# Kernel tuning notes

Hardware: AMD Instinct MI355X
Metric: run time of the kernel (lower is better)

## Reference

```python
import jax, jax.numpy as jnp
import numpy as np

B, S, D, H = 2, 2048, 1024, 16
HD = D // H

def setup_inputs() -> dict:
    key = jax.random.key(0)
    ks = jax.random.split(key, 11)
    s = 1.0 / np.sqrt(D)
    return {
        "query": jax.random.normal(ks[0], (B, S, D), jnp.float32),
        "key": jax.random.normal(ks[1], (B, S, D), jnp.float32),
        "value": jax.random.normal(ks[2], (B, S, D), jnp.float32),
        "Wq": jax.random.normal(ks[3], (D, D), jnp.float32) * s,
        "bq": jax.random.normal(ks[4], (D,), jnp.float32) * s,
        "Wk": jax.random.normal(ks[5], (D, D), jnp.float32) * s,
        "bk": jax.random.normal(ks[6], (D,), jnp.float32) * s,
        "Wv": jax.random.normal(ks[7], (D, D), jnp.float32) * s,
        "bv": jax.random.normal(ks[8], (D,), jnp.float32) * s,
        "Wo": jax.random.normal(ks[9], (D, D), jnp.float32) * s,
        "bo": jax.random.normal(ks[10], (D,), jnp.float32) * s,
        "test": 0,
    }

def _heads(x, W, b):
    # [B,S,D] @ [D,D] -> [B,S,D] -> [B,H,S,HD]
    y = x @ W + b
    return y.reshape(B, -1, H, HD).transpose(0, 2, 1, 3)

def reference(query, key, value, Wq, bq, Wk, bk, Wv, bv, Wo, bo, test):
    q = _heads(query, Wq, bq)
    k = _heads(key, Wk, bk)
    v = _heads(value, Wv, bv)
    scale = 1.0 / np.sqrt(HD).astype(np.float32)
    scores = jnp.einsum('bhqd,bhkd->bhqk', q, k) * scale  # [B,H,S,S]
    if test:
        return scores
    prob = jax.nn.softmax(scores, axis=-1)
    out = jnp.einsum('bhqk,bhkd->bhqd', prob, v)
    out = out.transpose(0, 2, 1, 3).reshape(B, -1, D)
    return out @ Wo + bo
```

## Files before the change

### kernel.cpp

```cpp
#include <hip/hip_runtime.h>

constexpr int Bn  = 2;
constexpr int Sn  = 2048;
constexpr int Dn  = 1024;
constexpr int Hn  = 16;
constexpr int HDn = 64;
constexpr int Mn  = Bn * Sn;

typedef _Float16 half8 __attribute__((ext_vector_type(8)));
typedef _Float16 half4 __attribute__((ext_vector_type(4)));
typedef float    f32x4 __attribute__((ext_vector_type(4)));

__device__ __forceinline__ void cp16(const _Float16* g, _Float16* l) {
  __builtin_amdgcn_global_load_lds(
      (__attribute__((address_space(1))) void*)g,
      (__attribute__((address_space(3))) void*)l, 16, 0, 0);
}

__global__ __launch_bounds__(256) void prep_kernel(
    const float* __restrict__ q, const float* __restrict__ k,
    const float* __restrict__ v,
    const float* __restrict__ Wq, const float* __restrict__ Wk,
    const float* __restrict__ Wv, const float* __restrict__ Wo,
    _Float16* __restrict__ Xh, _Float16* __restrict__ WT) {
  __shared__ float tile[64][65];
  const int n = blockIdx.x;
  const int tid = threadIdx.x;
  if (n < 12288) {
    const int z = n >> 12;
    const float* src = (z == 0) ? q : (z == 1) ? k : v;
    _Float16* dst = Xh + (size_t)z * (Mn * Dn);
    int i = (n & 4095) * 256 + tid;
    float4 v4 = ((const float4*)src)[i];
    half4 h;
    h.x = (_Float16)v4.x; h.y = (_Float16)v4.y;
    h.z = (_Float16)v4.z; h.w = (_Float16)v4.w;
    *(half4*)(dst + (size_t)i * 4) = h;
  } else {
    const int m = n - 12288;
    const int z = m >> 8, rem = m & 255;
    const float* W = (z == 0) ? Wq : (z == 1) ? Wk : (z == 2) ? Wv : Wo;
    _Float16* T = WT + (size_t)z * Dn * Dn;
    const int k0 = (rem >> 4) * 64, n0 = (rem & 15) * 64;
#pragma unroll
    for (int i = 0; i < 4; i++) {
      int s = tid + i * 256;
      int r = s >> 4, c4 = s & 15;
      float4 w4 = *(const float4*)(W + (size_t)(k0 + r) * Dn + n0 + c4 * 4);
      tile[r][c4 * 4 + 0] = w4.x; tile[r][c4 * 4 + 1] = w4.y;
      tile[r][c4 * 4 + 2] = w4.z; tile[r][c4 * 4 + 3] = w4.w;
    }
    __syncthreads();
#pragma unroll
    for (int i = 0; i < 2; i++) {
      int s = tid + i * 256;
      int nn = s >> 3, r8 = (s & 7) * 8;
      half8 h;
#pragma unroll
      for (int j = 0; j < 8; j++) h[j] = (_Float16)tile[r8 + j][nn];
      *(half8*)(T + (size_t)(n0 + nn) * Dn + k0 + r8) = h;
    }
  }
}

__global__ __launch_bounds__(256) void proj_kernel(
    const _Float16* __restrict__ Xh, const _Float16* __restrict__ WT,
    const float* __restrict__ bq, const float* __restrict__ bk,
    const float* __restrict__ bv,
    _Float16* __restrict__ Qh, _Float16* __restrict__ Kh,
    _Float16* __restrict__ VT) {
  const int z = blockIdx.z;
  const _Float16* A  = Xh + (size_t)z * Mn * Dn;
  const _Float16* Bm = WT + (size_t)z * Dn * Dn;
  const float* bias = (z == 0) ? bq : (z == 1) ? bk : bv;

  __shared__ __align__(16) _Float16 smem[2 * 128 * 64];
  _Float16* As = smem;
  _Float16* Bs = smem + 128 * 64;

  const int tid  = threadIdx.x;
  const int lane = tid & 63;
  const int w    = tid >> 6;
  const int wm   = (w >> 1) * 64;
  const int wn   = (w & 1) * 64;
  const int m0   = blockIdx.y * 128;
  const int n0   = blockIdx.x * 128;
  const int qd   = lane >> 4;
  const int lm   = lane & 15;

  const int st_r = tid >> 3;
  const int st_u = (tid & 7) ^ (st_r & 7);

  f32x4 acc[4][4];
#pragma unroll
  for (int i = 0; i < 4; i++)
#pragma unroll
    for (int j = 0; j < 4; j++) acc[i][j] = {0.f, 0.f, 0.f, 0.f};

  for (int k0 = 0; k0 < Dn; k0 += 64) {
#pragma unroll
    for (int p = 0; p < 4; p++) {
      int row = st_r + p * 32;
      cp16(A + (size_t)(m0 + row) * Dn + k0 + st_u * 8, As + (tid + p * 256) * 8);
      cp16(Bm + (size_t)(n0 + row) * Dn + k0 + st_u * 8, Bs + (tid + p * 256) * 8);
    }
    __syncthreads();
#pragma unroll
    for (int ks = 0; ks < 2; ks++) {
      const int up = ((ks * 4 + qd) ^ (lm & 7)) * 8;
      half8 a[4], bb[4];
#pragma unroll
      for (int mi = 0; mi < 4; mi++)
        a[mi] = *(const half8*)(As + (wm + mi * 16 + lm) * 64 + up);
#pragma unroll
      for (int ni = 0; ni < 4; ni++)
        bb[ni] = *(const half8*)(Bs + (wn + ni * 16 + lm) * 64 + up);
      if (z < 2) {
#pragma unroll
        for (int mi = 0; mi < 4; mi++)
#pragma unroll
          for (int ni = 0; ni < 4; ni++)
            acc[mi][ni] = __builtin_amdgcn_mfma_f32_16x16x32_f16(bb[ni], a[mi], acc[mi][ni], 0, 0, 0);
      } else {
#pragma unroll
        for (int mi = 0; mi < 4; mi++)
#pragma unroll
          for (int ni = 0; ni < 4; ni++)
            acc[mi][ni] = __builtin_amdgcn_mfma_f32_16x16x32_f16(a[mi], bb[ni], acc[mi][ni], 0, 0, 0);
      }
    }
    __syncthreads();
  }

  char* T = (char*)smem;
  const int b_ = m0 >> 11, s0 = m0 & (Sn - 1), h0 = n0 >> 6;

  if (z < 2) {
    _Float16* out = (z == 0) ? Qh : Kh;
    const float scl = (z == 0) ? 0.125f * 1.44269504089f : 1.0f;
#pragma unroll
    for (int mi = 0; mi < 4; mi++) {
      int tok = wm + mi * 16 + lm;
#pragma unroll
      for (int ni = 0; ni < 4; ni++) {
        int feat = wn + ni * 16 + qd * 4;
        float4 b4 = *(const float4*)(bias + n0 + feat);
        half4 h4;
        h4[0] = (_Float16)((acc[mi][ni][0] + b4.x) * scl);
        h4[1] = (_Float16)((acc[mi][ni][1] + b4.y) * scl);
        h4[2] = (_Float16)((acc[mi][ni][2] + b4.z) * scl);
        h4[3] = (_Float16)((acc[mi][ni][3] + b4.w) * scl);
        *(half4*)(T + tok * 256 + ((feat * 2) ^ ((tok & 7) << 4))) = h4;
      }
    }
    __syncthreads();
#pragma unroll
    for (int i = 0; i < 8; i++) {
      int slot = tid + i * 256;
      int r = slot >> 3, c16 = slot & 7;
      int hh = r >> 7, sm = r & 127;
      half8 v8 = *(const half8*)(T + sm * 256 + ((hh * 128 + c16 * 16) ^ ((sm & 7) << 4)));
      *(half8*)(out + (((size_t)(b_ * Hn + h0 + hh)) * Sn + s0 + sm) * HDn + c16 * 8) = v8;
    }
  } else {
#pragma unroll
    for (int ni = 0; ni < 4; ni++) {
      int feat = wn + ni * 16 + lm;
      float b_f = bias[n0 + feat];
#pragma unroll
      for (int mi = 0; mi < 4; mi++) {
        int tk = wm + mi * 16 + qd * 4;
        half4 h4;
#pragma unroll
        for (int r = 0; r < 4; r++) h4[r] = (_Float16)(acc[mi][ni][r] + b_f);
        *(half4*)(T + feat * 256 + ((tk * 2) ^ ((feat & 7) << 4))) = h4;
      }
    }
    __syncthreads();
#pragma unroll
    for (int i = 0; i < 8; i++) {
      int slot = tid + i * 256;
      int f = slot >> 4, c16 = slot & 15;
      half8 v8 = *(const half8*)(T + f * 256 + ((c16 * 16) ^ ((f & 7) << 4)));
      int head = h0 + (f >> 6), hd = f & 63;
      *(half8*)(VT + (((size_t)(b_ * Hn + head)) * HDn + hd) * Sn + s0 + c16 * 8) = v8;
    }
  }
}

__global__ __launch_bounds__(256, 2) void attn_kernel(
    const _Float16* __restrict__ Qh, const _Float16* __restrict__ Kh,
    const _Float16* __restrict__ VT, _Float16* __restrict__ attn_out) {
  __shared__ __align__(16) _Float16 Ksb[2][128 * 64];
  __shared__ __align__(16) _Float16 Vsb[2][64 * 128];
  __shared__ __align__(16) _Float16 Ps[4 * 32 * 64];

  const int n    = blockIdx.x;
  const int slot = n >> 3;
  const int bh   = (n & 7) * 4 + (slot >> 4);
  const int q0   = (slot & 15) * 128;
  const size_t base = (size_t)bh * Sn * HDn;

  const int tid  = threadIdx.x;
  const int lane = tid & 63;
  const int w    = tid >> 6;
  const int qd   = lane >> 4;
  const int lm   = lane & 15;

  const _Float16* qptr = Qh + base + (size_t)(q0 + w * 32 + lm) * HDn + qd * 8;
  half8 qa[2][2];
#pragma unroll
  for (int nj = 0; nj < 2; nj++)
#pragma unroll
    for (int ks = 0; ks < 2; ks++)
      qa[nj][ks] = *(const half8*)(qptr + nj * 16 * HDn + ks * 32);

  half8 vones;
#pragma unroll
  for (int j = 0; j < 8; j++) vones[j] = (lm == 0) ? (_Float16)1.0f : (_Float16)0.0f;

  f32x4 oacc[2][4];
#pragma unroll
  for (int i = 0; i < 2; i++)
#pragma unroll
    for (int j = 0; j < 4; j++) oacc[i][j] = {0.f, 0.f, 0.f, 0.f};
  f32x4 oaccl[2] = {{0.f, 0.f, 0.f, 0.f}, {0.f, 0.f, 0.f, 0.f}};

  char* Psw = (char*)(Ps + w * (32 * 64));
  const f32x4 sinit = {-10.f, -10.f, -10.f, -10.f};

  const int st_r = tid >> 3;
  const int st_u = (tid & 7) ^ (st_r & 7);
  const _Float16* kbase = Kh + base;
  const _Float16* vbase = VT + base;

#define STAGE_K(KT, DST)                                                     \
  {                                                                          \
    const _Float16* src_ = kbase + (size_t)(KT) * 128 * HDn;                 \
    _Float16* dst_ = (DST);                                                  \
    _Pragma("unroll")                                                        \
    for (int p = 0; p < 4; p++)                                              \
      cp16(src_ + (size_t)(st_r + p * 32) * HDn + st_u * 8,                  \
           dst_ + (tid + p * 256) * 8);                                      \
  }

#define STAGE_V(KT, DST)                                                     \
  {                                                                          \
    _Float16* dst_ = (DST);                                                  \
    _Pragma("unroll")                                                        \
    for (int p = 0; p < 4; p++) {                                            \
      int s_ = tid + p * 256;                                                \
      int r_ = s_ >> 4, u_ = (s_ & 15) ^ (r_ & 15);                          \
      cp16(vbase + (size_t)r_ * Sn + (KT) * 128 + u_ * 8, dst_ + s_ * 8);    \
    }                                                                        \
  }

#define LOAD_V(C, VB)                                                        \
  _Pragma("unroll")                                                          \
  for (int oi = 0; oi < 4; oi++)                                             \
    _Pragma("unroll")                                                        \
    for (int k2 = 0; k2 < 2; k2++)                                           \
      VB[oi][k2] = *(const half8*)(Vsb[cur] +                                \
          ((oi * 16 + lm) * 16 + (((C) * 8 + k2 * 4 + qd) ^ lm)) * 8);

#define QK(C, SACC)                                                          \
  {                                                                          \
    _Pragma("unroll")                                                        \
    for (int n4 = 0; n4 < 4; n4++)                                           \
      _Pragma("unroll")                                                      \
      for (int nj = 0; nj < 2; nj++) SACC[n4][nj] = sinit;                   \
    __builtin_amdgcn_s_setprio(1);                                           \
    _Pragma("unroll")                                                        \
    for (int n4 = 0; n4 < 4; n4++) {                                         \
      int ni = 4 * (C) + n4;                                                 \
      _Pragma("unroll")                                                      \
      for (int ks = 0; ks < 2; ks++) {                                       \
        int up = (4 * ks + qd) ^ (lm & 7);                                   \
        half8 ka = *(const half8*)(Ksb[cur] + (ni * 16 + lm) * HDn + up * 8);\
        _Pragma("unroll")                                                    \
        for (int nj = 0; nj < 2; nj++)                                       \
          SACC[n4][nj] = __builtin_amdgcn_mfma_f32_16x16x32_f16(             \
              ka, qa[nj][ks], SACC[n4][nj], 0, 0, 0);                        \
      }                                                                      \
    }                                                                        \
    __builtin_amdgcn_s_setprio(0);                                           \
  }

#define SM(SACC)                                                             \
  _Pragma("unroll")                                                          \
  for (int nj = 0; nj < 2; nj++)                                             \
    _Pragma("unroll")                                                        \
    for (int n4 = 0; n4 < 4; n4++) {                                         \
      float p0 = __builtin_amdgcn_exp2f(SACC[n4][nj][0]);                    \
      float p1 = __builtin_amdgcn_exp2f(SACC[n4][nj][1]);                    \
      float p2 = __builtin_amdgcn_exp2f(SACC[n4][nj][2]);                    \
      float p3 = __builtin_amdgcn_exp2f(SACC[n4][nj][3]);                    \
      auto lo = __builtin_amdgcn_cvt_pkrtz(p0, p1);                          \
      auto hi = __builtin_amdgcn_cvt_pkrtz(p2, p3);                          \
      half4 h4;                                                              \
      h4[0] = (_Float16)lo[0]; h4[1] = (_Float16)lo[1];                      \
      h4[2] = (_Float16)hi[0]; h4[3] = (_Float16)hi[1];                      \
      *(half4*)(Psw + (nj * 16 + lm) * 128 +                                 \
                ((n4 * 32 + qd * 8) ^ ((lm & 7) << 4))) = h4;                \
    }

#define PV(VB)                                                               \
  _Pragma("unroll")                                                          \
  for (int k2 = 0; k2 < 2; k2++) {                                           \
    half8 pa[2];                                                             \
    _Pragma("unroll")                                                        \
    for (int mi = 0; mi < 2; mi++)                                           \
      pa[mi] = *(const half8*)(Psw + (mi * 16 + lm) * 128 +                  \
                               ((k2 * 64 + qd * 16) ^ ((lm & 7) << 4)));     \
    __builtin_amdgcn_s_setprio(1);                                           \
    _Pragma("unroll")                                                        \
    for (int oi = 0; oi < 4; oi++)                                           \
      _Pragma("unroll")                                                      \
      for (int mi = 0; mi < 2; mi++)                                         \
        oacc[mi][oi] = __builtin_amdgcn_mfma_f32_16x16x32_f16(               \
            VB[oi][k2], pa[mi], oacc[mi][oi], 0, 0, 0);                      \
    _Pragma("unroll")                                                        \
    for (int mi = 0; mi < 2; mi++)                                           \
      oaccl[mi] = __builtin_amdgcn_mfma_f32_16x16x32_f16(                    \
          vones, pa[mi], oaccl[mi], 0, 0, 0);                                \
    __builtin_amdgcn_s_setprio(0);                                           \
  }

  STAGE_K(0, Ksb[0])
  STAGE_V(0, Vsb[0])
  __syncthreads();

  int cur = 0;
  for (int kt = 0; kt < Sn / 128; kt++) {
    if (kt + 1 < Sn / 128) {
      STAGE_K(kt + 1, Ksb[cur ^ 1])
      STAGE_V(kt + 1, Vsb[cur ^ 1])
    }

    f32x4 sacc[2][4][2];
    half8 vbA[4][2], vbB[4][2];

    LOAD_V(0, vbA)
    QK(0, sacc[0])
    QK(1, sacc[1])
    SM(sacc[0])
    LOAD_V(1, vbB)
    PV(vbA)
    SM(sacc[1])
    PV(vbB)

    __syncthreads();
    cur ^= 1;
  }
#undef STAGE_K
#undef STAGE_V
#undef LOAD_V
#undef QK
#undef SM
#undef PV

  const int b_ = bh >> 4, h_ = bh & 15;
#pragma unroll
  for (int mi = 0; mi < 2; mi++) {
    float lr = __shfl(oaccl[mi][0], lm, 64);
    float inv = 1.0f / lr;
    int qrow = q0 + w * 32 + mi * 16 + lm;
    size_t rowbase = ((size_t)(b_ * Sn + qrow)) * Dn + h_ * 64;
#pragma unroll
    for (int oi = 0; oi < 4; oi++) {
      half4 h4;
#pragma unroll
      for (int r = 0; r < 4; r++) h4[r] = (_Float16)(oacc[mi][oi][r] * inv);
      *(half4*)(attn_out + rowbase + oi * 16 + qd * 4) = h4;
    }
  }
}

__global__ __launch_bounds__(256) void outproj_kernel(
    const _Float16* __restrict__ Aattn, const _Float16* __restrict__ WoT,
    const float* __restrict__ bo, float* __restrict__ out) {
  __shared__ __align__(16) _Float16 smem[(64 + 128) * 128];
  _Float16* As = smem;
  _Float16* Bs = smem + 64 * 128;

  const int tid  = threadIdx.x;
  const int lane = tid & 63;
  const int w    = tid >> 6;
  const int wm   = (w >> 1) * 32;
  const int wn   = (w & 1) * 64;
  const int m0   = blockIdx.y * 64;
  const int n0   = blockIdx.x * 128;
  const int qd   = lane >> 4;
  const int lm   = lane & 15;

  f32x4 acc[2][4];
#pragma unroll
  for (int i = 0; i < 2; i++)
#pragma unroll
    for (int j = 0; j < 4; j++) acc[i][j] = {0.f, 0.f, 0.f, 0.f};

  for (int k0 = 0; k0 < Dn; k0 += 128) {
#pragma unroll
    for (int p = 0; p < 4; p++) {
      int s = tid + p * 256;
      int r = s >> 4, u = (s & 15) ^ (r & 15);
      cp16(Aattn + (size_t)(m0 + r) * Dn + k0 + u * 8, As + s * 8);
    }
#pragma unroll
    for (int p = 0; p < 8; p++) {
      int s = tid + p * 256;
      int r = s >> 4, u = (s & 15) ^ (r & 15);
      cp16(WoT + (size_t)(n0 + r) * Dn + k0 + u * 8, Bs + s * 8);
    }
    __syncthreads();
#pragma unroll
    for (int ks = 0; ks < 4; ks++) {
      const int up = (ks * 4 + qd) ^ lm;
      half8 a[2], bb[4];
#pragma unroll
      for (int mi = 0; mi < 2; mi++)
        a[mi] = *(const half8*)(As + ((wm + mi * 16 + lm) * 16 + up) * 8);
#pragma unroll
      for (int ni = 0; ni < 4; ni++)
        bb[ni] = *(const half8*)(Bs + ((wn + ni * 16 + lm) * 16 + up) * 8);
#pragma unroll
      for (int mi = 0; mi < 2; mi++)
#pragma unroll
        for (int ni = 0; ni < 4; ni++)
          acc[mi][ni] = __builtin_amdgcn_mfma_f32_16x16x32_f16(bb[ni], a[mi], acc[mi][ni], 0, 0, 0);
    }
    __syncthreads();
  }

  float* T = (float*)smem;
#pragma unroll
  for (int mi = 0; mi < 2; mi++) {
    int m = wm + mi * 16 + lm;
#pragma unroll
    for (int ni = 0; ni < 4; ni++) {
      int nb = wn + ni * 16 + qd * 4;
      float4 b4 = *(const float4*)(bo + n0 + nb);
      f32x4 o;
      o[0] = acc[mi][ni][0] + b4.x;
      o[1] = acc[mi][ni][1] + b4.y;
      o[2] = acc[mi][ni][2] + b4.z;
      o[3] = acc[mi][ni][3] + b4.w;
      *(f32x4*)((char*)T + m * 512 + ((nb * 4) ^ ((m & 7) << 4))) = o;
    }
  }
  __syncthreads();
#pragma unroll
  for (int i = 0; i < 8; i++) {
    int s = tid + i * 256;
    int r = s >> 5, c = s & 31;
    f32x4 v = *(const f32x4*)((char*)T + r * 512 + ((c * 16) ^ ((r & 7) << 4)));
    *(f32x4*)(out + (size_t)(m0 + r) * Dn + n0 + c * 4) = v;
  }
}

extern "C" void kernel_launch(void* const* d_in, const int* in_sizes, int n_in,
                              void* d_out, int out_size, void* d_ws, size_t ws_size,
                              hipStream_t stream) {
  const float* query = (const float*)d_in[0];
  const float* key_  = (const float*)d_in[1];
  const float* value = (const float*)d_in[2];
  const float* Wq = (const float*)d_in[3];
  const float* bq = (const float*)d_in[4];
  const float* Wk = (const float*)d_in[5];
  const float* bk = (const float*)d_in[6];
  const float* Wv = (const float*)d_in[7];
  const float* bv = (const float*)d_in[8];
  const float* Wo = (const float*)d_in[9];
  const float* bo = (const float*)d_in[10];

  _Float16* Xh = (_Float16*)d_ws;
  _Float16* WT = Xh + (size_t)3 * Mn * Dn;
  _Float16* Qh = WT + (size_t)4 * Dn * Dn;
  _Float16* Kh = Qh + (size_t)Mn * Dn;
  _Float16* VT = Kh + (size_t)Mn * Dn;
  _Float16* attnb = Xh;
  float* out = (float*)d_out;

  dim3 blk(256);
  prep_kernel<<<dim3(12288 + 1024), blk, 0, stream>>>(
      query, key_, value, Wq, Wk, Wv, Wo, Xh, WT);
  proj_kernel<<<dim3(Dn / 128, Mn / 128, 3), blk, 0, stream>>>(
      Xh, WT, bq, bk, bv, Qh, Kh, VT);
  attn_kernel<<<dim3(512), blk, 0, stream>>>(Qh, Kh, VT, attnb);
  outproj_kernel<<<dim3(Dn / 128, Mn / 64), blk, 0, stream>>>(
      attnb, WT + (size_t)3 * Dn * Dn, bo, out);
}
```

Baseline: 224.7 us.

## Split attention work across 8 waves with 16 query rows per wave

The attention kernel now runs 512 threads (8 waves) per block instead of 4, and each wave handles 16 query rows instead of 32. Per-wave accumulators, Q fragments and the P scratch shrink, and K/V staging is spread over twice as many threads. The aim is more waves in flight to hide LDS and softmax latency and lower register pressure. In exchange, every K and V fragment read from LDS now feeds half as many MFMAs, so LDS traffic per FLOP doubles.

Measured after the change: 262.1 us. +16.6%, slower.

```diff
diff --git a/kernel.cpp b/kernel.cpp
--- a/kernel.cpp
+++ b/kernel.cpp
@@ -188,12 +188,12 @@
   }
 }
 
-__global__ __launch_bounds__(256, 2) void attn_kernel(
+__global__ __launch_bounds__(512, 4) void attn_kernel(
     const _Float16* __restrict__ Qh, const _Float16* __restrict__ Kh,
     const _Float16* __restrict__ VT, _Float16* __restrict__ attn_out) {
   __shared__ __align__(16) _Float16 Ksb[2][128 * 64];
   __shared__ __align__(16) _Float16 Vsb[2][64 * 128];
-  __shared__ __align__(16) _Float16 Ps[4 * 32 * 64];
+  __shared__ __align__(16) _Float16 Ps[8 * 16 * 64];
 
   const int n    = blockIdx.x;
   const int slot = n >> 3;
@@ -207,30 +207,24 @@
   const int qd   = lane >> 4;
   const int lm   = lane & 15;
 
-  const _Float16* qptr = Qh + base + (size_t)(q0 + w * 32 + lm) * HDn + qd * 8;
-  half8 qa[2][2];
-#pragma unroll
-  for (int nj = 0; nj < 2; nj++)
-#pragma unroll
-    for (int ks = 0; ks < 2; ks++)
-      qa[nj][ks] = *(const half8*)(qptr + nj * 16 * HDn + ks * 32);
+  const _Float16* qptr = Qh + base + (size_t)(q0 + w * 16 + lm) * HDn + qd * 8;
+  half8 qa[2];
+#pragma unroll
+  for (int ks = 0; ks < 2; ks++)
+    qa[ks] = *(const half8*)(qptr + ks * 32);
 
   half8 vones;
 #pragma unroll
   for (int j = 0; j < 8; j++) vones[j] = (lm == 0) ? (_Float16)1.0f : (_Float16)0.0f;
 
-  f32x4 oacc[2][4];
-#pragma unroll
-  for (int i = 0; i < 2; i++)
-#pragma unroll
-    for (int j = 0; j < 4; j++) oacc[i][j] = {0.f, 0.f, 0.f, 0.f};
-  f32x4 oaccl[2] = {{0.f, 0.f, 0.f, 0.f}, {0.f, 0.f, 0.f, 0.f}};
-
-  char* Psw = (char*)(Ps + w * (32 * 64));
+  f32x4 oacc[4];
+#pragma unroll
+  for (int j = 0; j < 4; j++) oacc[j] = {0.f, 0.f, 0.f, 0.f};
+  f32x4 oaccl = {0.f, 0.f, 0.f, 0.f};
+
+  char* Psw = (char*)(Ps + w * (16 * 64));
   const f32x4 sinit = {-10.f, -10.f, -10.f, -10.f};
 
-  const int st_r = tid >> 3;
-  const int st_u = (tid & 7) ^ (st_r & 7);
   const _Float16* kbase = Kh + base;
   const _Float16* vbase = VT + base;
 
@@ -239,17 +233,19 @@
     const _Float16* src_ = kbase + (size_t)(KT) * 128 * HDn;                 \
     _Float16* dst_ = (DST);                                                  \
     _Pragma("unroll")                                                        \
-    for (int p = 0; p < 4; p++)                                              \
-      cp16(src_ + (size_t)(st_r + p * 32) * HDn + st_u * 8,                  \
-           dst_ + (tid + p * 256) * 8);                                      \
+    for (int p = 0; p < 2; p++) {                                            \
+      int s_ = tid + p * 512;                                                \
+      int r_ = s_ >> 3, u_ = (s_ & 7) ^ (r_ & 7);                            \
+      cp16(src_ + (size_t)r_ * HDn + u_ * 8, dst_ + s_ * 8);                 \
+    }                                                                        \
   }
 
 #define STAGE_V(KT, DST)                                                     \
   {                                                                          \
     _Float16* dst_ = (DST);                                                  \
     _Pragma("unroll")                                                        \
-    for (int p = 0; p < 4; p++) {                                            \
-      int s_ = tid + p * 256;                                                \
+    for (int p = 0; p < 2; p++) {                                            \
+      int s_ = tid + p * 512;                                                \
       int r_ = s_ >> 4, u_ = (s_ & 15) ^ (r_ & 15);                          \
       cp16(vbase + (size_t)r_ * Sn + (KT) * 128 + u_ * 8, dst_ + s_ * 8);    \
     }                                                                        \
@@ -266,9 +262,7 @@
 #define QK(C, SACC)                                                          \
   {                                                                          \
     _Pragma("unroll")                                                        \
-    for (int n4 = 0; n4 < 4; n4++)                                           \
-      _Pragma("unroll")                                                      \
-      for (int nj = 0; nj < 2; nj++) SACC[n4][nj] = sinit;                   \
+    for (int n4 = 0; n4 < 4; n4++) SACC[n4] = sinit;                         \
     __builtin_amdgcn_s_setprio(1);                                           \
     _Pragma("unroll")                                                        \
     for (int n4 = 0; n4 < 4; n4++) {                                         \
@@ -277,10 +271,8 @@
       for (int ks = 0; ks < 2; ks++) {                                       \
         int up = (4 * ks + qd) ^ (lm & 7);                                   \
         half8 ka = *(const half8*)(Ksb[cur] + (ni * 16 + lm) * HDn + up * 8);\
-        _Pragma("unroll")                                                    \
-        for (int nj = 0; nj < 2; nj++)                                       \
-          SACC[n4][nj] = __builtin_amdgcn_mfma_f32_16x16x32_f16(             \
-              ka, qa[nj][ks], SACC[n4][nj], 0, 0, 0);                        \
+        SACC[n4] = __builtin_amdgcn_mfma_f32_16x16x32_f16(                   \
+            ka, qa[ks], SACC[n4], 0, 0, 0);                                  \
       }                                                                      \
     }                                                                        \
     __builtin_amdgcn_s_setprio(0);                                           \
@@ -288,41 +280,31 @@
 
 #define SM(SACC)                                                             \
   _Pragma("unroll")                                                          \
-  for (int nj = 0; nj < 2; nj++)                                             \
-    _Pragma("unroll")                                                        \
-    for (int n4 = 0; n4 < 4; n4++) {                                         \
-      float p0 = __builtin_amdgcn_exp2f(SACC[n4][nj][0]);                    \
-      float p1 = __builtin_amdgcn_exp2f(SACC[n4][nj][1]);                    \
-      float p2 = __builtin_amdgcn_exp2f(SACC[n4][nj][2]);                    \
-      float p3 = __builtin_amdgcn_exp2f(SACC[n4][nj][3]);                    \
-      auto lo = __builtin_amdgcn_cvt_pkrtz(p0, p1);                          \
-      auto hi = __builtin_amdgcn_cvt_pkrtz(p2, p3);                          \
-      half4 h4;                                                              \
-      h4[0] = (_Float16)lo[0]; h4[1] = (_Float16)lo[1];                      \
-      h4[2] = (_Float16)hi[0]; h4[3] = (_Float16)hi[1];                      \
-      *(half4*)(Psw + (nj * 16 + lm) * 128 +                                 \
-                ((n4 * 32 + qd * 8) ^ ((lm & 7) << 4))) = h4;                \
-    }
+  for (int n4 = 0; n4 < 4; n4++) {                                           \
+    float p0 = __builtin_amdgcn_exp2f(SACC[n4][0]);                          \
+    float p1 = __builtin_amdgcn_exp2f(SACC[n4][1]);                          \
+    float p2 = __builtin_amdgcn_exp2f(SACC[n4][2]);                          \
+    float p3 = __builtin_amdgcn_exp2f(SACC[n4][3]);                          \
+    auto lo = __builtin_amdgcn_cvt_pkrtz(p0, p1);                            \
+    auto hi = __builtin_amdgcn_cvt_pkrtz(p2, p3);                            \
+    half4 h4;                                                                \
+    h4[0] = (_Float16)lo[0]; h4[1] = (_Float16)lo[1];                        \
+    h4[2] = (_Float16)hi[0]; h4[3] = (_Float16)hi[1];                        \
+    *(half4*)(Psw + lm * 128 + ((n4 * 32 + qd * 8) ^ ((lm & 7) << 4))) = h4; \
+  }
 
 #define PV(VB)                                                               \
   _Pragma("unroll")                                                          \
   for (int k2 = 0; k2 < 2; k2++) {                                           \
-    half8 pa[2];                                                             \
-    _Pragma("unroll")                                                        \
-    for (int mi = 0; mi < 2; mi++)                                           \
-      pa[mi] = *(const half8*)(Psw + (mi * 16 + lm) * 128 +                  \
+    half8 pa = *(const half8*)(Psw + lm * 128 +                              \
                                ((k2 * 64 + qd * 16) ^ ((lm & 7) << 4)));     \
     __builtin_amdgcn_s_setprio(1);                                           \
     _Pragma("unroll")                                                        \
     for (int oi = 0; oi < 4; oi++)                                           \
-      _Pragma("unroll")                                                      \
-      for (int mi = 0; mi < 2; mi++)                                         \
-        oacc[mi][oi] = __builtin_amdgcn_mfma_f32_16x16x32_f16(               \
-            VB[oi][k2], pa[mi], oacc[mi][oi], 0, 0, 0);                      \
-    _Pragma("unroll")                                                        \
-    for (int mi = 0; mi < 2; mi++)                                           \
-      oaccl[mi] = __builtin_amdgcn_mfma_f32_16x16x32_f16(                    \
-          vones, pa[mi], oaccl[mi], 0, 0, 0);                                \
+      oacc[oi] = __builtin_amdgcn_mfma_f32_16x16x32_f16(                     \
+          VB[oi][k2], pa, oacc[oi], 0, 0, 0);                                \
+    oaccl = __builtin_amdgcn_mfma_f32_16x16x32_f16(                          \
+        vones, pa, oaccl, 0, 0, 0);                                          \
     __builtin_amdgcn_s_setprio(0);                                           \
   }
 
@@ -337,7 +319,7 @@
       STAGE_V(kt + 1, Vsb[cur ^ 1])
     }
 
-    f32x4 sacc[2][4][2];
+    f32x4 sacc[2][4];
     half8 vbA[4][2], vbB[4][2];
 
     LOAD_V(0, vbA)
@@ -360,19 +342,16 @@
 #undef PV
 
   const int b_ = bh >> 4, h_ = bh & 15;
-#pragma unroll
-  for (int mi = 0; mi < 2; mi++) {
-    float lr = __shfl(oaccl[mi][0], lm, 64);
-    float inv = 1.0f / lr;
-    int qrow = q0 + w * 32 + mi * 16 + lm;
-    size_t rowbase = ((size_t)(b_ * Sn + qrow)) * Dn + h_ * 64;
-#pragma unroll
-    for (int oi = 0; oi < 4; oi++) {
-      half4 h4;
-#pragma unroll
-      for (int r = 0; r < 4; r++) h4[r] = (_Float16)(oacc[mi][oi][r] * inv);
-      *(half4*)(attn_out + rowbase + oi * 16 + qd * 4) = h4;
-    }
+  float lr = __shfl(oaccl[0], lm, 64);
+  float inv = 1.0f / lr;
+  int qrow = q0 + w * 16 + lm;
+  size_t rowbase = ((size_t)(b_ * Sn + qrow)) * Dn + h_ * 64;
+#pragma unroll
+  for (int oi = 0; oi < 4; oi++) {
+    half4 h4;
+#pragma unroll
+    for (int r = 0; r < 4; r++) h4[r] = (_Float16)(oacc[oi][r] * inv);
+    *(half4*)(attn_out + rowbase + oi * 16 + qd * 4) = h4;
   }
 }
 
@@ -486,7 +465,7 @@
       query, key_, value, Wq, Wk, Wv, Wo, Xh, WT);
   proj_kernel<<<dim3(Dn / 128, Mn / 128, 3), blk, 0, stream>>>(
       Xh, WT, bq, bk, bv, Qh, Kh, VT);
-  attn_kernel<<<dim3(512), blk, 0, stream>>>(Qh, Kh, VT, attnb);
+  attn_kernel<<<dim3(512), dim3(512), 0, stream>>>(Qh, Kh, VT, attnb);
   outproj_kernel<<<dim3(Dn / 128, Mn / 64), blk, 0, stream>>>(
       attnb, WT + (size_t)3 * Dn * Dn, bo, out);
 }
```
